# Kernel tuning notes

Hardware: AMD Instinct MI355X
Metric: run time of the kernel (lower is better)

## Reference

```python
import jax, jax.numpy as jnp
import numpy as np

EPS = 1e-12  # matches torch F.normalize default eps

def setup_inputs() -> dict:
    key = jax.random.key(0)
    k1, k2 = jax.random.split(key)
    n, d = 8192, 1024
    x = jax.random.normal(k1, (n, d), dtype=jnp.float32)
    weight = jax.random.normal(k2, (d, d), dtype=jnp.float32) * (2.0 / d) ** 0.5
    return {"x": x, "weight": weight}

def reference(x, weight):
    # L2-normalize rows (torch F.normalize, dim=1): x / max(||x||_2, eps)
    nrm = jnp.sqrt(jnp.sum(x * x, axis=1, keepdims=True))
    norm = x / jnp.maximum(nrm, EPS)
    # adjacency: cosine-similarity Gram matrix [n, n] (materialized as in source)
    adj = norm @ norm.T
    ax = adj @ x          # [n, d]
    axw = ax @ weight     # [n, d]
    return axw
```

## Files before the change

kernel.cpp:

```cpp
#include <hip/hip_runtime.h>
#include <stdint.h>

typedef unsigned short u16;
typedef unsigned int u32;
typedef __attribute__((ext_vector_type(8))) short short8;
typedef __attribute__((ext_vector_type(4))) float floatx4;

__device__ __forceinline__ u16 f2b(float f) {
    u32 u = __builtin_bit_cast(u32, f);
    return (u16)((u + 0x7fffu + ((u >> 16) & 1u)) >> 16);
}

__device__ __forceinline__ void gld16(const void* g, void* l) {
    __builtin_amdgcn_global_load_lds(
        (const __attribute__((address_space(1))) u32*)g,
        (__attribute__((address_space(3))) u32*)l, 16, 0, 0);
}

#define BARM() { asm volatile("" ::: "memory"); __builtin_amdgcn_s_barrier(); asm volatile("" ::: "memory"); }
#define VMCNT(n) asm volatile("s_waitcnt vmcnt(" #n ")" ::: "memory")

__global__ __launch_bounds__(256) void prep_all(
    const float* __restrict__ x, const float* __restrict__ wgt,
    u16* __restrict__ YT, u16* __restrict__ Yn, u16* __restrict__ Wt) {
    __shared__ __align__(16) float sh[16 * 1024];
    int b = blockIdx.x;
    int t = threadIdx.x;
    if (b < 512) {
        int r0 = b * 16;
        int tg = t >> 5, tl = t & 31;
        float ss[2] = {0.f, 0.f};
        for (int c = 0; c < 8; c++) {
            #pragma unroll
            for (int i = 0; i < 2; i++) {
                int row = i * 8 + tg;
                int col = c * 128 + tl * 4;
                float4 v = *(const float4*)(x + (long)(r0 + row) * 1024 + col);
                ss[i] += v.x * v.x + v.y * v.y + v.z * v.z + v.w * v.w;
                *(float4*)&sh[row * 1024 + (col ^ (row & 12))] = v;
            }
        }
        float sr_[2];
        #pragma unroll
        for (int i = 0; i < 2; i++) {
            #pragma unroll
            for (int m = 16; m > 0; m >>= 1) ss[i] += __shfl_xor(ss[i], m);
            float rcp = 1.0f / fmaxf(sqrtf(ss[i]), 1e-12f);
            sr_[i] = sqrtf(rcp);
        }
        for (int c = 0; c < 8; c++) {
            #pragma unroll
            for (int i = 0; i < 2; i++) {
                int row = i * 8 + tg;
                int col = c * 128 + tl * 4;
                float* p = &sh[row * 1024 + (col ^ (row & 12))];
                float4 v = *(float4*)p;
                v.x *= sr_[i]; v.y *= sr_[i]; v.z *= sr_[i]; v.w *= sr_[i];
                *(float4*)p = v;
                ushort4 o;
                o.x = f2b(v.x * sr_[i]); o.y = f2b(v.y * sr_[i]);
                o.z = f2b(v.z * sr_[i]); o.w = f2b(v.w * sr_[i]);
                *(ushort4*)(Yn + (long)(r0 + row) * 1024 + col) = o;
            }
        }
        __syncthreads();
        #pragma unroll
        for (int it = 0; it < 16; it++) {
            int lin = it * 256 + t;
            int cc = lin >> 2;
            int r4 = (lin & 3) << 2;
            ushort4 o;
            o.x = f2b(sh[(r4 + 0) * 1024 + (cc ^ r4)]);
            o.y = f2b(sh[(r4 + 1) * 1024 + (cc ^ r4)]);
            o.z = f2b(sh[(r4 + 2) * 1024 + (cc ^ r4)]);
            o.w = f2b(sh[(r4 + 3) * 1024 + (cc ^ r4)]);
            *(ushort4*)(YT + (long)cc * 8192 + r0 + r4) = o;
        }
    } else {
        float (*tile)[65] = (float(*)[65])sh;
        int bb = b - 512;
        int r0 = (bb >> 4) * 64, c0 = (bb & 15) * 64;
        #pragma unroll
        for (int i = 0; i < 4; i++) {
            int lin = i * 256 + t;
            int rr = lin >> 4, c4 = (lin & 15) << 2;
            float4 v = *(const float4*)(wgt + (long)(r0 + rr) * 1024 + c0 + c4);
            tile[rr][c4] = v.x; tile[rr][c4 + 1] = v.y;
            tile[rr][c4 + 2] = v.z; tile[rr][c4 + 3] = v.w;
        }
        __syncthreads();
        #pragma unroll
        for (int i = 0; i < 4; i++) {
            int lin = i * 256 + t;
            int cc = lin >> 4, r4 = (lin & 15) << 2;
            ushort4 o;
            o.x = f2b(tile[r4][cc]);
            o.y = f2b(tile[r4 + 1][cc]);
            o.z = f2b(tile[r4 + 2][cc]);
            o.w = f2b(tile[r4 + 3][cc]);
            *(ushort4*)(Wt + (long)(c0 + cc) * 1024 + r0 + r4) = o;
        }
    }
}

__global__ __launch_bounds__(256) void reduce_symC(
    const float* __restrict__ P, u16* __restrict__ D, int S, long E) {
    __shared__ float lt[64][65];
    int ti = blockIdx.x >> 4, tj = blockIdx.x & 15;
    if (ti > 2 * (tj >> 1) + 1) return;
    int mir = (tj > 2 * (ti >> 1) + 1);
    int t = threadIdx.x;
    int r = t >> 4, c4 = (t & 15) << 2;
    #pragma unroll
    for (int it = 0; it < 4; it++) {
        int row = it * 16 + r;
        long idx = (long)(64 * ti + row) * 1024 + 64 * tj + c4;
        float4 s = *(const float4*)(P + idx);
        for (int z = 1; z < S; z++) {
            float4 v = *(const float4*)(P + (long)z * E + idx);
            s.x += v.x; s.y += v.y; s.z += v.z; s.w += v.w;
        }
        ushort4 o; o.x = f2b(s.x); o.y = f2b(s.y); o.z = f2b(s.z); o.w = f2b(s.w);
        *(ushort4*)(D + idx) = o;
        if (mir) {
            lt[row][c4] = s.x; lt[row][c4 + 1] = s.y;
            lt[row][c4 + 2] = s.z; lt[row][c4 + 3] = s.w;
        }
    }
    if (mir) {
        __syncthreads();
        #pragma unroll
        for (int it = 0; it < 4; it++) {
            int dr = it * 16 + r;
            ushort4 o;
            o.x = f2b(lt[c4 + 0][dr]); o.y = f2b(lt[c4 + 1][dr]);
            o.z = f2b(lt[c4 + 2][dr]); o.w = f2b(lt[c4 + 3][dr]);
            *(ushort4*)(D + (long)(64 * tj + dr) * 1024 + 64 * ti + c4) = o;
        }
    }
}

__global__ __launch_bounds__(256, 3) void gemm64x128(
    const u16* __restrict__ A, const u16* __restrict__ B,
    float* __restrict__ C, const float* __restrict__ rowscale,
    int lda, int ldb, int ldc, int tilesN, int kIters, long coffz, int sym, int obf16) {
    __shared__ __align__(16) u16 As[2][64 * 64];
    __shared__ __align__(16) u16 Bs[2][128 * 64];
    int bid = blockIdx.x;
    int nx = gridDim.x;
    if ((nx & 7) == 0) { int cpx = nx >> 3; bid = (bid & 7) * cpx + (bid >> 3); }
    int tm, tn;
    if (sym) {
        int id = bid, j = 0;
        while (true) {
            int c = (2 * j + 2 < 16) ? (2 * j + 2) : 16;
            if (id < c) break;
            id -= c; j++;
        }
        tn = j; tm = id;
    } else {
        tm = bid / tilesN; tn = bid % tilesN;
    }
    long kOff = (long)blockIdx.y * kIters * 64;
    const u16* Ap = A + (long)tm * 64 * lda + kOff;
    const u16* Bp = B + (long)tn * 128 * ldb + kOff;
    long coff = (long)blockIdx.y * coffz;

    int t = threadIdx.x;
    int lane = t & 63, w = t >> 6;
    int wm = (w & 1) * 32, wn = (w >> 1) * 64;
    int r16 = lane & 15, q = lane >> 4;

    int acl[2], bcl[4];
    #pragma unroll
    for (int j = 0; j < 2; j++) acl[j] = (w * 2 + j) * 64 + lane;
    #pragma unroll
    for (int j = 0; j < 4; j++) bcl[j] = (w * 4 + j) * 64 + lane;

    floatx4 acc[2][4];
    #pragma unroll
    for (int i = 0; i < 2; i++)
        #pragma unroll
        for (int j = 0; j < 4; j++) acc[i][j] = (floatx4){0.f, 0.f, 0.f, 0.f};

    #define STAGE64(buf, kt)                                                    \
        {                                                                       \
            long kk = (long)(kt) * 64;                                          \
            _Pragma("unroll")                                                   \
            for (int j = 0; j < 2; j++) {                                       \
                int cl = acl[j], row = cl >> 3, cg = (cl & 7) ^ (row & 7);      \
                gld16(Ap + (long)row * lda + kk + cg * 8, (void*)&As[buf][cl * 8]); \
            }                                                                   \
            _Pragma("unroll")                                                   \
            for (int j = 0; j < 4; j++) {                                       \
                int cl = bcl[j], row = cl >> 3, cg = (cl & 7) ^ (row & 7);      \
                gld16(Bp + (long)row * ldb + kk + cg * 8, (void*)&Bs[buf][cl * 8]); \
            }                                                                   \
        }

    #define COMPUTE64(buf)                                                      \
        {                                                                       \
            _Pragma("unroll")                                                   \
            for (int ks = 0; ks < 2; ks++) {                                    \
                short8 a[2], b[4];                                              \
                _Pragma("unroll")                                               \
                for (int i = 0; i < 2; i++) {                                   \
                    int rr = wm + i * 16 + r16;                                 \
                    int cc = (ks * 4 + q) ^ (rr & 7);                           \
                    a[i] = *(const short8*)&As[buf][rr * 64 + cc * 8];          \
                }                                                               \
                _Pragma("unroll")                                               \
                for (int j = 0; j < 4; j++) {                                   \
                    int rr = wn + j * 16 + r16;                                 \
                    int cc = (ks * 4 + q) ^ (rr & 7);                           \
                    b[j] = *(const short8*)&Bs[buf][rr * 64 + cc * 8];          \
                }                                                               \
                _Pragma("unroll")                                               \
                for (int i = 0; i < 2; i++)                                     \
                    _Pragma("unroll")                                           \
                    for (int j = 0; j < 4; j++)                                 \
                        acc[i][j] = __builtin_amdgcn_mfma_f32_16x16x32_bf16(    \
                            a[i], b[j], acc[i][j], 0, 0, 0);                    \
            }                                                                   \
        }

    STAGE64(0, 0);
    STAGE64(1, 1);
    VMCNT(6);
    BARM();
    int cur = 0;
    for (int kt = 0; kt < kIters - 2; kt++) {
        COMPUTE64(cur);
        BARM();
        STAGE64(cur, kt + 2);
        VMCNT(6);
        BARM();
        cur ^= 1;
    }
    COMPUTE64(cur);
    VMCNT(0);
    BARM();
    COMPUTE64(cur ^ 1);

    int m0 = tm * 64 + wm, n0 = tn * 128 + wn;
    #pragma unroll
    for (int i = 0; i < 2; i++) {
        int mm = m0 + i * 16 + q * 4;
        float rs[4];
        #pragma unroll
        for (int r = 0; r < 4; r++) rs[r] = (rowscale != nullptr) ? rowscale[mm + r] : 1.0f;
        #pragma unroll
        for (int j = 0; j < 4; j++) {
            int nn = n0 + j * 16 + r16;
            #pragma unroll
            for (int r = 0; r < 4; r++) {
                float v = acc[i][j][r] * rs[r];
                if (obf16) ((u16*)C)[coff + (long)(mm + r) * ldc + nn] = f2b(v);
                else       C[coff + (long)(mm + r) * ldc + nn] = v;
            }
        }
    }
    #undef STAGE64
    #undef COMPUTE64
}

__global__ __launch_bounds__(256, 2) void gemm128(
    const u16* __restrict__ A, const u16* __restrict__ B,
    float* __restrict__ C, const float* __restrict__ rowscale,
    int lda, int ldb, int ldc, int tilesN, int kIters) {
    __shared__ __align__(16) u16 As[2][128 * 64];
    __shared__ __align__(16) u16 Bs[2][128 * 64];
    int bid = blockIdx.x;
    int nx = gridDim.x;
    if ((nx & 7) == 0) { int cpx = nx >> 3; bid = (bid & 7) * cpx + (bid >> 3); }
    int tm = bid / tilesN, tn = bid % tilesN;
    const u16* Ap = A + (long)tm * 128 * lda;
    const u16* Bp = B + (long)tn * 128 * ldb;

    int t = threadIdx.x;
    int lane = t & 63, w = t >> 6;
    int wm = (w & 1) * 64, wn = (w >> 1) * 64;
    int r16 = lane & 15, q = lane >> 4;

    floatx4 acc[4][4];
    #pragma unroll
    for (int i = 0; i < 4; i++)
        #pragma unroll
        for (int j = 0; j < 4; j++) acc[i][j] = (floatx4){0.f, 0.f, 0.f, 0.f};

    #define STAGE128(buf, kt)                                                   \
        {                                                                       \
            long kk = (long)(kt) * 64;                                          \
            _Pragma("unroll")                                                   \
            for (int j = 0; j < 4; j++) {                                       \
                int cl = j * 256 + t, row = cl >> 3, cg = (cl & 7) ^ (row & 7); \
                gld16(Ap + (long)row * lda + kk + cg * 8, (void*)&As[buf][cl * 8]); \
            }                                                                   \
            _Pragma("unroll")                                                   \
            for (int j = 0; j < 4; j++) {                                       \
                int cl = j * 256 + t, row = cl >> 3, cg = (cl & 7) ^ (row & 7); \
                gld16(Bp + (long)row * ldb + kk + cg * 8, (void*)&Bs[buf][cl * 8]); \
            }                                                                   \
        }

    #define COMPUTE128(buf)                                                     \
        {                                                                       \
            _Pragma("unroll")                                                   \
            for (int ks = 0; ks < 2; ks++) {                                    \
                short8 a[4], b[4];                                              \
                _Pragma("unroll")                                               \
                for (int i = 0; i < 4; i++) {                                   \
                    int rr = wm + i * 16 + r16;                                 \
                    int cc = (ks * 4 + q) ^ (rr & 7);                           \
                    a[i] = *(const short8*)&As[buf][rr * 64 + cc * 8];          \
                }                                                               \
                _Pragma("unroll")                                               \
                for (int j = 0; j < 4; j++) {                                   \
                    int rr = wn + j * 16 + r16;                                 \
                    int cc = (ks * 4 + q) ^ (rr & 7);                           \
                    b[j] = *(const short8*)&Bs[buf][rr * 64 + cc * 8];          \
                }                                                               \
                _Pragma("unroll")                                               \
                for (int i = 0; i < 4; i++)                                     \
                    _Pragma("unroll")                                           \
                    for (int j = 0; j < 4; j++)                                 \
                        acc[i][j] = __builtin_amdgcn_mfma_f32_16x16x32_bf16(    \
                            a[i], b[j], acc[i][j], 0, 0, 0);                    \
            }                                                                   \
        }

    STAGE128(0, 0);
    STAGE128(1, 1);
    VMCNT(8);
    BARM();
    int cur = 0;
    for (int kt = 0; kt < kIters - 2; kt++) {
        COMPUTE128(cur);
        BARM();
        STAGE128(cur, kt + 2);
        VMCNT(8);
        BARM();
        cur ^= 1;
    }
    COMPUTE128(cur);
    VMCNT(0);
    BARM();
    COMPUTE128(cur ^ 1);

    int m0 = tm * 128 + wm, n0 = tn * 128 + wn;
    #pragma unroll
    for (int i = 0; i < 4; i++) {
        int mm = m0 + i * 16 + q * 4;
        float rs[4];
        #pragma unroll
        for (int r = 0; r < 4; r++) rs[r] = (rowscale != nullptr) ? rowscale[mm + r] : 1.0f;
        #pragma unroll
        for (int j = 0; j < 4; j++) {
            int nn = n0 + j * 16 + r16;
            #pragma unroll
            for (int r = 0; r < 4; r++)
                C[(long)(mm + r) * ldc + nn] = acc[i][j][r] * rs[r];
        }
    }
    #undef STAGE128
    #undef COMPUTE128
}

extern "C" void kernel_launch(void* const* d_in, const int* in_sizes, int n_in,
                              void* d_out, int out_size, void* d_ws, size_t ws_size,
                              hipStream_t stream) {
    const float* x = (const float*)d_in[0];
    const float* wgt = (const float*)d_in[1];
    float* out = (float*)d_out;
    char* ws = (char*)d_ws;

    const size_t MB = 1048576;
    u16*   YT = (u16*)ws;
    u16*   Yn = (u16*)(ws + 16 * MB);
    u16*   Wt = (u16*)(ws + 32 * MB);
    u16*   Gb = (u16*)(ws + 34 * MB);
    u16*   Mt = (u16*)(ws + 36 * MB);
    float* Gp = (float*)(ws + 38 * MB);

    prep_all<<<768, 256, 0, stream>>>(x, wgt, YT, Yn, Wt);
    gemm64x128<<<dim3(72, 8), 256, 0, stream>>>(YT, YT, Gp, nullptr,
                                                8192, 8192, 1024, 8, 16, 1048576, 1, 0);
    reduce_symC<<<256, 256, 0, stream>>>(Gp, Gb, 8, 1048576);
    gemm64x128<<<dim3(128, 1), 256, 0, stream>>>(Wt, Gb, (float*)Mt, nullptr,
                                                 1024, 1024, 1024, 8, 16, 0, 0, 1);
    gemm128<<<dim3(512, 1), 256, 0, stream>>>(Yn, Mt, out, nullptr,
                                              1024, 1024, 1024, 8, 16);
}
```

Before: 152.8 us.

## Enlarge final GEMM tile to 256x128 and split-K the small weight GEMM

The final Yn·Mt GEMM now uses 256x128 tiles with 8x4 MFMA accumulators per wave. This halves the block count to 256, one per CU, and raises operand reuse per LDS load, at the cost of lower occupancy and higher register pressure. The 1024x1024 Wt·Gb GEMM is split along K into two halves written as fp32 partials, then summed and cast to bf16 by a new reduce_cast kernel, to get more parallelism for that small GEMM. This adds an extra kernel launch and partial-buffer traffic.

```diff
diff --git a/kernel.cpp b/kernel.cpp
--- a/kernel.cpp
+++ b/kernel.cpp
@@ -140,6 +140,19 @@
     }
 }
 
+__global__ __launch_bounds__(256) void reduce_cast(
+    const float* __restrict__ P, u16* __restrict__ D, int S, long E) {
+    long i = ((long)blockIdx.x * 256 + threadIdx.x) * 4;
+    float4 s = *(const float4*)(P + i);
+    for (int z = 1; z < S; z++) {
+        float4 v = *(const float4*)(P + z * E + i);
+        s.x += v.x; s.y += v.y; s.z += v.z; s.w += v.w;
+    }
+    ushort4 o;
+    o.x = f2b(s.x); o.y = f2b(s.y); o.z = f2b(s.z); o.w = f2b(s.w);
+    *(ushort4*)(D + i) = o;
+}
+
 __global__ __launch_bounds__(256, 3) void gemm64x128(
     const u16* __restrict__ A, const u16* __restrict__ B,
     float* __restrict__ C, const float* __restrict__ rowscale,
@@ -264,52 +277,51 @@
     #undef COMPUTE64
 }
 
-__global__ __launch_bounds__(256, 2) void gemm128(
+__global__ __launch_bounds__(256, 1) void gemm256x128(
     const u16* __restrict__ A, const u16* __restrict__ B,
-    float* __restrict__ C, const float* __restrict__ rowscale,
-    int lda, int ldb, int ldc, int tilesN, int kIters) {
-    __shared__ __align__(16) u16 As[2][128 * 64];
+    float* __restrict__ C, int lda, int ldb, int ldc, int tilesN, int kIters) {
+    __shared__ __align__(16) u16 As[2][256 * 64];
     __shared__ __align__(16) u16 Bs[2][128 * 64];
     int bid = blockIdx.x;
     int nx = gridDim.x;
     if ((nx & 7) == 0) { int cpx = nx >> 3; bid = (bid & 7) * cpx + (bid >> 3); }
     int tm = bid / tilesN, tn = bid % tilesN;
-    const u16* Ap = A + (long)tm * 128 * lda;
+    const u16* Ap = A + (long)tm * 256 * lda;
     const u16* Bp = B + (long)tn * 128 * ldb;
 
     int t = threadIdx.x;
     int lane = t & 63, w = t >> 6;
-    int wm = (w & 1) * 64, wn = (w >> 1) * 64;
+    int wm = (w & 1) * 128, wn = (w >> 1) * 64;
     int r16 = lane & 15, q = lane >> 4;
 
-    floatx4 acc[4][4];
-    #pragma unroll
-    for (int i = 0; i < 4; i++)
+    floatx4 acc[8][4];
+    #pragma unroll
+    for (int i = 0; i < 8; i++)
         #pragma unroll
         for (int j = 0; j < 4; j++) acc[i][j] = (floatx4){0.f, 0.f, 0.f, 0.f};
 
-    #define STAGE128(buf, kt)                                                   \
+    #define STAGE256(buf, kt)                                                   \
         {                                                                       \
             long kk = (long)(kt) * 64;                                          \
             _Pragma("unroll")                                                   \
-            for (int j = 0; j < 4; j++) {                                       \
+            for (int j = 0; j < 8; j++) {    \
                 int cl = j * 256 + t, row = cl >> 3, cg = (cl & 7) ^ (row & 7); \
                 gld16(Ap + (long)row * lda + kk + cg * 8, (void*)&As[buf][cl * 8]); \
             }                                                                   \
             _Pragma("unroll")                                                   \
-            for (int j = 0; j < 4; j++) {                                       \
+            for (int j = 0; j < 4; j++) {    \
                 int cl = j * 256 + t, row = cl >> 3, cg = (cl & 7) ^ (row & 7); \
                 gld16(Bp + (long)row * ldb + kk + cg * 8, (void*)&Bs[buf][cl * 8]); \
             }                                                                   \
         }
 
-    #define COMPUTE128(buf)                                                     \
+    #define COMPUTE256(buf)                                                     \
         {                                                                       \
             _Pragma("unroll")                                                   \
             for (int ks = 0; ks < 2; ks++) {                                    \
-                short8 a[4], b[4];                                              \
-                _Pragma("unroll")                                               \
-                for (int i = 0; i < 4; i++) {                                   \
+                short8 a[8], b[4];                                              \
+                _Pragma("unroll")                                               \
+                for (int i = 0; i < 8; i++) {                                   \
                     int rr = wm + i * 16 + r16;                                 \
                     int cc = (ks * 4 + q) ^ (rr & 7);                           \
                     a[i] = *(const short8*)&As[buf][rr * 64 + cc * 8];          \
@@ -321,7 +333,7 @@
                     b[j] = *(const short8*)&Bs[buf][rr * 64 + cc * 8];          \
                 }                                                               \
                 _Pragma("unroll")                                               \
-                for (int i = 0; i < 4; i++)                                     \
+                for (int i = 0; i < 8; i++)                                     \
                     _Pragma("unroll")                                           \
                     for (int j = 0; j < 4; j++)                                 \
                         acc[i][j] = __builtin_amdgcn_mfma_f32_16x16x32_bf16(    \
@@ -329,41 +341,38 @@
             }                                                                   \
         }
 
-    STAGE128(0, 0);
-    STAGE128(1, 1);
-    VMCNT(8);
+    STAGE256(0, 0);
+    STAGE256(1, 1);
+    VMCNT(12);
     BARM();
     int cur = 0;
     for (int kt = 0; kt < kIters - 2; kt++) {
-        COMPUTE128(cur);
+        COMPUTE256(cur);
         BARM();
-        STAGE128(cur, kt + 2);
-        VMCNT(8);
+        STAGE256(cur, kt + 2);
+        VMCNT(12);
         BARM();
         cur ^= 1;
     }
-    COMPUTE128(cur);
+    COMPUTE256(cur);
     VMCNT(0);
     BARM();
-    COMPUTE128(cur ^ 1);
-
-    int m0 = tm * 128 + wm, n0 = tn * 128 + wn;
-    #pragma unroll
-    for (int i = 0; i < 4; i++) {
+    COMPUTE256(cur ^ 1);
+
+    int m0 = tm * 256 + wm, n0 = tn * 128 + wn;
+    #pragma unroll
+    for (int i = 0; i < 8; i++) {
         int mm = m0 + i * 16 + q * 4;
-        float rs[4];
-        #pragma unroll
-        for (int r = 0; r < 4; r++) rs[r] = (rowscale != nullptr) ? rowscale[mm + r] : 1.0f;
         #pragma unroll
         for (int j = 0; j < 4; j++) {
             int nn = n0 + j * 16 + r16;
             #pragma unroll
             for (int r = 0; r < 4; r++)
-                C[(long)(mm + r) * ldc + nn] = acc[i][j][r] * rs[r];
-        }
-    }
-    #undef STAGE128
-    #undef COMPUTE128
+                C[(long)(mm + r) * ldc + nn] = acc[i][j][r];
+        }
+    }
+    #undef STAGE256
+    #undef COMPUTE256
 }
 
 extern "C" void kernel_launch(void* const* d_in, const int* in_sizes, int n_in,
@@ -381,13 +390,15 @@
     u16*   Gb = (u16*)(ws + 34 * MB);
     u16*   Mt = (u16*)(ws + 36 * MB);
     float* Gp = (float*)(ws + 38 * MB);
+    float* Mp = (float*)(ws + 70 * MB);
 
     prep_all<<<768, 256, 0, stream>>>(x, wgt, YT, Yn, Wt);
     gemm64x128<<<dim3(72, 8), 256, 0, stream>>>(YT, YT, Gp, nullptr,
                                                 8192, 8192, 1024, 8, 16, 1048576, 1, 0);
     reduce_symC<<<256, 256, 0, stream>>>(Gp, Gb, 8, 1048576);
-    gemm64x128<<<dim3(128, 1), 256, 0, stream>>>(Wt, Gb, (float*)Mt, nullptr,
-                                                 1024, 1024, 1024, 8, 16, 0, 0, 1);
-    gemm128<<<dim3(512, 1), 256, 0, stream>>>(Yn, Mt, out, nullptr,
-                                              1024, 1024, 1024, 8, 16);
-}
+    gemm64x128<<<dim3(128, 2), 256, 0, stream>>>(Wt, Gb, Mp, nullptr,
+                                                 1024, 1024, 1024, 8, 8, 1048576, 0, 0);
+    reduce_cast<<<1024, 256, 0, stream>>>(Mp, Mt, 2, 1048576);
+    gemm256x128<<<dim3(256, 1), 256, 0, stream>>>(Yn, Mt, out,
+                                                  1024, 1024, 1024, 8, 16);
+}
```

Result: slower. 161.2 us (+5.5%).
